# Kernel optimization log

Hardware: AMD Instinct MI355X
Metric: run time of the kernel (lower is better)

Reference implementation:

```python
import jax, jax.numpy as jnp
import numpy as np

N = 10000
E = 320000
F_IN = 512
NHID = 32
LATENT = 16


def setup_inputs() -> dict:
    key = jax.random.key(0)
    k1, k2, k3, k4, k5 = jax.random.split(key, 5)
    x = jax.random.normal(k1, (N, F_IN), dtype=jnp.float32)
    W1 = jax.random.normal(k2, (F_IN, NHID), dtype=jnp.float32) * (1.0 / np.sqrt(F_IN))
    W2 = jax.random.normal(k3, (NHID, LATENT), dtype=jnp.float32) * (1.0 / np.sqrt(NHID))
    edge_index = jax.random.randint(k4, (2, E), 0, N, dtype=jnp.int32)
    edge_weight = jax.random.uniform(k5, (E,), dtype=jnp.float32)
    return {"x": x, "W1": W1, "W2": W2, "edge_index": edge_index,
            "edge_weight": edge_weight}


def _spmm(edge_index, edge_weight, h):
    # out[dst] += w * h[src]  (sparse normalized-adjacency matmul)
    src, dst = edge_index[0], edge_index[1]
    msgs = edge_weight[:, None] * h[src]          # [E, D] gather + scale
    return jax.ops.segment_sum(msgs, dst, num_segments=N)  # [N, D]


def reference(x, W1, W2, edge_index, edge_weight):
    # GCNConv layer 1: adj @ (x @ W1)
    h = _spmm(edge_index, edge_weight, x @ W1)    # [N, NHID]
    # GCNConv layer 2: adj @ (h @ W2)
    z = _spmm(edge_index, edge_weight, h @ W2)    # [N, LATENT]
    # Inner-product decoder: sigmoid(z @ z^T)
    adj_recon = jax.nn.sigmoid(z @ z.T)           # [N, N]
    return adj_recon, z
```

## Files before the change

### kernel.cpp

```cpp
#include <hip/hip_runtime.h>
#include <cstdint>
#include <cstddef>

#define N_NODES 10000
#define F_IN    512
#define NHID    32
#define LATENT  16

__global__ __launch_bounds__(256) void gemm1_kernel(const float* __restrict__ x,
                                                    const float* __restrict__ W1,
                                                    float* __restrict__ h0) {
    __shared__ float xs[8][F_IN];
    const int row0 = blockIdx.x * 8;
    for (int t = threadIdx.x; t < 8 * F_IN; t += 256) {
        const int r = t >> 9;
        const int c = t & (F_IN - 1);
        if (row0 + r < N_NODES)
            xs[r][c] = x[(size_t)(row0 + r) * F_IN + c];
    }
    __syncthreads();

    const int col = threadIdx.x & 31;
    const int r   = threadIdx.x >> 5;
    if (row0 + r < N_NODES) {
        float acc = 0.f;
#pragma unroll 8
        for (int k = 0; k < F_IN; ++k) {
            acc += xs[r][k] * W1[k * NHID + col];
        }
        h0[(size_t)(row0 + r) * NHID + col] = acc;
    }
}

template <int D>
__global__ __launch_bounds__(256) void spmm_kernel(const int* __restrict__ src,
                                                   const int* __restrict__ dst,
                                                   const float* __restrict__ w,
                                                   const float* __restrict__ hin,
                                                   float* __restrict__ hout,
                                                   int E) {
    const int idx = blockIdx.x * 256 + threadIdx.x;
    const int e = idx / D;
    const int d = idx & (D - 1);
    if (e < E) {
        const int s = src[e];
        const int t = dst[e];
        const float val = w[e] * hin[(size_t)s * D + d];
        atomicAdd(&hout[(size_t)t * D + d], val);
    }
}

__global__ __launch_bounds__(256) void gemm2_kernel(const float* __restrict__ h,
                                                    const float* __restrict__ W2,
                                                    float* __restrict__ z0) {
    __shared__ float w2s[NHID * LATENT];
    for (int t = threadIdx.x; t < NHID * LATENT; t += 256) w2s[t] = W2[t];
    __syncthreads();

    const int idx = blockIdx.x * 256 + threadIdx.x;
    if (idx < N_NODES * LATENT) {
        const int row = idx >> 4;
        const int col = idx & (LATENT - 1);
        const float* __restrict__ hr = h + (size_t)row * NHID;
        float acc = 0.f;
#pragma unroll
        for (int k = 0; k < NHID; ++k) acc += hr[k] * w2s[k * LATENT + col];
        z0[idx] = acc;
    }
}

#define TI 32

__device__ __forceinline__ float sigmoid_fast(float x) {
    return __builtin_amdgcn_rcpf(1.0f + __expf(-x));
}

__global__ __launch_bounds__(256) void decoder_kernel(const float* __restrict__ z,
                                                      float* __restrict__ out) {
    const int j  = blockIdx.x * 256 + threadIdx.x;
    const int i0 = blockIdx.y * TI;

    float4 zj0, zj1, zj2, zj3;
    if (j < N_NODES) {
        const float4* __restrict__ zp = (const float4*)(z + (size_t)j * LATENT);
        zj0 = zp[0]; zj1 = zp[1]; zj2 = zp[2]; zj3 = zp[3];
    } else {
        zj0 = zj1 = zj2 = zj3 = make_float4(0.f, 0.f, 0.f, 0.f);
    }

    const int imax = min(TI, N_NODES - i0);
    if (imax == TI) {
#pragma unroll 4
        for (int ii = 0; ii < TI; ++ii) {
            const float4* __restrict__ zi = (const float4*)(z + (size_t)(i0 + ii) * LATENT);
            const float4 a0 = zi[0], a1 = zi[1], a2 = zi[2], a3 = zi[3];
            float acc = a0.x * zj0.x + a0.y * zj0.y + a0.z * zj0.z + a0.w * zj0.w
                      + a1.x * zj1.x + a1.y * zj1.y + a1.z * zj1.z + a1.w * zj1.w
                      + a2.x * zj2.x + a2.y * zj2.y + a2.z * zj2.z + a2.w * zj2.w
                      + a3.x * zj3.x + a3.y * zj3.y + a3.z * zj3.z + a3.w * zj3.w;
            if (j < N_NODES) {
                __builtin_nontemporal_store(sigmoid_fast(acc),
                                            &out[(size_t)(i0 + ii) * N_NODES + j]);
            }
        }
    } else {
        for (int ii = 0; ii < imax; ++ii) {
            const float4* __restrict__ zi = (const float4*)(z + (size_t)(i0 + ii) * LATENT);
            const float4 a0 = zi[0], a1 = zi[1], a2 = zi[2], a3 = zi[3];
            float acc = a0.x * zj0.x + a0.y * zj0.y + a0.z * zj0.z + a0.w * zj0.w
                      + a1.x * zj1.x + a1.y * zj1.y + a1.z * zj1.z + a1.w * zj1.w
                      + a2.x * zj2.x + a2.y * zj2.y + a2.z * zj2.z + a2.w * zj2.w
                      + a3.x * zj3.x + a3.y * zj3.y + a3.z * zj3.z + a3.w * zj3.w;
            if (j < N_NODES) {
                __builtin_nontemporal_store(sigmoid_fast(acc),
                                            &out[(size_t)(i0 + ii) * N_NODES + j]);
            }
        }
    }
}

extern "C" void kernel_launch(void* const* d_in, const int* in_sizes, int n_in,
                              void* d_out, int out_size, void* d_ws, size_t ws_size,
                              hipStream_t stream) {
    const float* x  = (const float*)d_in[0];
    const float* W1 = (const float*)d_in[1];
    const float* W2 = (const float*)d_in[2];
    const int*   ei = (const int*)d_in[3];
    const float* ew = (const float*)d_in[4];
    const int E = in_sizes[3] / 2;
    const int* src = ei;
    const int* dst = ei + E;

    float* out = (float*)d_out;
    float* z   = out + (size_t)N_NODES * N_NODES;

    float* h0 = out;
    float* h  = h0 + N_NODES * NHID;
    float* z0 = h  + N_NODES * NHID;

    hipMemsetAsync(h, 0, (size_t)N_NODES * NHID * sizeof(float), stream);
    hipMemsetAsync(z, 0, (size_t)N_NODES * LATENT * sizeof(float), stream);

    gemm1_kernel<<<(N_NODES + 7) / 8, 256, 0, stream>>>(x, W1, h0);
    spmm_kernel<NHID><<<(E * NHID + 255) / 256, 256, 0, stream>>>(src, dst, ew, h0, h, E);

    gemm2_kernel<<<(N_NODES * LATENT + 255) / 256, 256, 0, stream>>>(h, W2, z0);
    spmm_kernel<LATENT><<<(E * LATENT + 255) / 256, 256, 0, stream>>>(src, dst, ew, z0, z, E);

    dim3 dgrid((N_NODES + 255) / 256, (N_NODES + TI - 1) / TI);
    decoder_kernel<<<dgrid, 256, 0, stream>>>(z, out);
}
```

Before: 507.9 us.

## Fold memsets into gemm1, vectorize decoder stores to four columns per thread

Removes the two hipMemsetAsync calls and zeroes the spmm accumulators inside gemm1, using one thread per element across the 1250 blocks. gemm1 now reads x from shared memory as float4 and keeps four independent accumulators. The decoder computes four output columns per thread and writes them with one 128-bit nontemporal store per row, which cuts per-thread z_i loads and store instructions for the dominant 400MB output write. Bounds checks are dropped because N is divisible by 8 and by 4.

```diff
diff --git a/kernel.cpp b/kernel.cpp
--- a/kernel.cpp
+++ b/kernel.cpp
@@ -7,29 +7,38 @@
 #define NHID    32
 #define LATENT  16
 
+typedef float v4f __attribute__((ext_vector_type(4)));
+
 __global__ __launch_bounds__(256) void gemm1_kernel(const float* __restrict__ x,
                                                     const float* __restrict__ W1,
-                                                    float* __restrict__ h0) {
+                                                    float* __restrict__ h0,
+                                                    float* __restrict__ h,
+                                                    float* __restrict__ z) {
+    const int gid = blockIdx.x * 256 + threadIdx.x;
+    h[gid] = 0.f;
+    if (gid < N_NODES * LATENT) z[gid] = 0.f;
+
     __shared__ float xs[8][F_IN];
     const int row0 = blockIdx.x * 8;
     for (int t = threadIdx.x; t < 8 * F_IN; t += 256) {
         const int r = t >> 9;
         const int c = t & (F_IN - 1);
-        if (row0 + r < N_NODES)
-            xs[r][c] = x[(size_t)(row0 + r) * F_IN + c];
+        xs[r][c] = x[(size_t)(row0 + r) * F_IN + c];
     }
     __syncthreads();
 
     const int col = threadIdx.x & 31;
     const int r   = threadIdx.x >> 5;
-    if (row0 + r < N_NODES) {
-        float acc = 0.f;
-#pragma unroll 8
-        for (int k = 0; k < F_IN; ++k) {
-            acc += xs[r][k] * W1[k * NHID + col];
-        }
-        h0[(size_t)(row0 + r) * NHID + col] = acc;
+    float a0 = 0.f, a1 = 0.f, a2 = 0.f, a3 = 0.f;
+#pragma unroll 4
+    for (int k = 0; k < F_IN; k += 4) {
+        const float4 xv = *(const float4*)&xs[r][k];
+        a0 += xv.x * W1[(k + 0) * NHID + col];
+        a1 += xv.y * W1[(k + 1) * NHID + col];
+        a2 += xv.z * W1[(k + 2) * NHID + col];
+        a3 += xv.w * W1[(k + 3) * NHID + col];
     }
+    h0[(size_t)(row0 + r) * NHID + col] = (a0 + a1) + (a2 + a3);
 }
 
 template <int D>
@@ -77,45 +86,53 @@
 
 __global__ __launch_bounds__(256) void decoder_kernel(const float* __restrict__ z,
                                                       float* __restrict__ out) {
-    const int j  = blockIdx.x * 256 + threadIdx.x;
+    const int j0 = (blockIdx.x * 256 + threadIdx.x) << 2;
     const int i0 = blockIdx.y * TI;
+    if (j0 >= N_NODES) return;
 
-    float4 zj0, zj1, zj2, zj3;
-    if (j < N_NODES) {
-        const float4* __restrict__ zp = (const float4*)(z + (size_t)j * LATENT);
-        zj0 = zp[0]; zj1 = zp[1]; zj2 = zp[2]; zj3 = zp[3];
-    } else {
-        zj0 = zj1 = zj2 = zj3 = make_float4(0.f, 0.f, 0.f, 0.f);
+    float4 zj0[4], zj1[4], zj2[4], zj3[4];
+    {
+        const float4* zp0 = (const float4*)(z + (size_t)(j0 + 0) * LATENT);
+        const float4* zp1 = (const float4*)(z + (size_t)(j0 + 1) * LATENT);
+        const float4* zp2 = (const float4*)(z + (size_t)(j0 + 2) * LATENT);
+        const float4* zp3 = (const float4*)(z + (size_t)(j0 + 3) * LATENT);
+#pragma unroll
+        for (int p = 0; p < 4; ++p) {
+            zj0[p] = zp0[p]; zj1[p] = zp1[p]; zj2[p] = zp2[p]; zj3[p] = zp3[p];
+        }
     }
 
     const int imax = min(TI, N_NODES - i0);
-    if (imax == TI) {
-#pragma unroll 4
-        for (int ii = 0; ii < TI; ++ii) {
-            const float4* __restrict__ zi = (const float4*)(z + (size_t)(i0 + ii) * LATENT);
-            const float4 a0 = zi[0], a1 = zi[1], a2 = zi[2], a3 = zi[3];
-            float acc = a0.x * zj0.x + a0.y * zj0.y + a0.z * zj0.z + a0.w * zj0.w
-                      + a1.x * zj1.x + a1.y * zj1.y + a1.z * zj1.z + a1.w * zj1.w
-                      + a2.x * zj2.x + a2.y * zj2.y + a2.z * zj2.z + a2.w * zj2.w
-                      + a3.x * zj3.x + a3.y * zj3.y + a3.z * zj3.z + a3.w * zj3.w;
-            if (j < N_NODES) {
-                __builtin_nontemporal_store(sigmoid_fast(acc),
-                                            &out[(size_t)(i0 + ii) * N_NODES + j]);
-            }
-        }
-    } else {
-        for (int ii = 0; ii < imax; ++ii) {
-            const float4* __restrict__ zi = (const float4*)(z + (size_t)(i0 + ii) * LATENT);
-            const float4 a0 = zi[0], a1 = zi[1], a2 = zi[2], a3 = zi[3];
-            float acc = a0.x * zj0.x + a0.y * zj0.y + a0.z * zj0.z + a0.w * zj0.w
-                      + a1.x * zj1.x + a1.y * zj1.y + a1.z * zj1.z + a1.w * zj1.w
-                      + a2.x * zj2.x + a2.y * zj2.y + a2.z * zj2.z + a2.w * zj2.w
-                      + a3.x * zj3.x + a3.y * zj3.y + a3.z * zj3.z + a3.w * zj3.w;
-            if (j < N_NODES) {
-                __builtin_nontemporal_store(sigmoid_fast(acc),
-                                            &out[(size_t)(i0 + ii) * N_NODES + j]);
-            }
-        }
+#pragma unroll 2
+    for (int ii = 0; ii < imax; ++ii) {
+        const float4* __restrict__ zi = (const float4*)(z + (size_t)(i0 + ii) * LATENT);
+        const float4 a0 = zi[0], a1 = zi[1], a2 = zi[2], a3 = zi[3];
+
+        v4f r;
+        r.x = a0.x*zj0[0].x + a0.y*zj0[0].y + a0.z*zj0[0].z + a0.w*zj0[0].w
+            + a1.x*zj0[1].x + a1.y*zj0[1].y + a1.z*zj0[1].z + a1.w*zj0[1].w
+            + a2.x*zj0[2].x + a2.y*zj0[2].y + a2.z*zj0[2].z + a2.w*zj0[2].w
+            + a3.x*zj0[3].x + a3.y*zj0[3].y + a3.z*zj0[3].z + a3.w*zj0[3].w;
+        r.y = a0.x*zj1[0].x + a0.y*zj1[0].y + a0.z*zj1[0].z + a0.w*zj1[0].w
+            + a1.x*zj1[1].x + a1.y*zj1[1].y + a1.z*zj1[1].z + a1.w*zj1[1].w
+            + a2.x*zj1[2].x + a2.y*zj1[2].y + a2.z*zj1[2].z + a2.w*zj1[2].w
+            + a3.x*zj1[3].x + a3.y*zj1[3].y + a3.z*zj1[3].z + a3.w*zj1[3].w;
+        r.z = a0.x*zj2[0].x + a0.y*zj2[0].y + a0.z*zj2[0].z + a0.w*zj2[0].w
+            + a1.x*zj2[1].x + a1.y*zj2[1].y + a1.z*zj2[1].z + a1.w*zj2[1].w
+            + a2.x*zj2[2].x + a2.y*zj2[2].y + a2.z*zj2[2].z + a2.w*zj2[2].w
+            + a3.x*zj2[3].x + a3.y*zj2[3].y + a3.z*zj2[3].z + a3.w*zj2[3].w;
+        r.w = a0.x*zj3[0].x + a0.y*zj3[0].y + a0.z*zj3[0].z + a0.w*zj3[0].w
+            + a1.x*zj3[1].x + a1.y*zj3[1].y + a1.z*zj3[1].z + a1.w*zj3[1].w
+            + a2.x*zj3[2].x + a2.y*zj3[2].y + a2.z*zj3[2].z + a2.w*zj3[2].w
+            + a3.x*zj3[3].x + a3.y*zj3[3].y + a3.z*zj3[3].z + a3.w*zj3[3].w;
+
+        r.x = sigmoid_fast(r.x);
+        r.y = sigmoid_fast(r.y);
+        r.z = sigmoid_fast(r.z);
+        r.w = sigmoid_fast(r.w);
+
+        __builtin_nontemporal_store(
+            r, (v4f*)(out + (size_t)(i0 + ii) * N_NODES + j0));
     }
 }
 
@@ -138,15 +155,12 @@
     float* h  = h0 + N_NODES * NHID;
     float* z0 = h  + N_NODES * NHID;
 
-    hipMemsetAsync(h, 0, (size_t)N_NODES * NHID * sizeof(float), stream);
-    hipMemsetAsync(z, 0, (size_t)N_NODES * LATENT * sizeof(float), stream);
-
-    gemm1_kernel<<<(N_NODES + 7) / 8, 256, 0, stream>>>(x, W1, h0);
+    gemm1_kernel<<<N_NODES / 8, 256, 0, stream>>>(x, W1, h0, h, z);
     spmm_kernel<NHID><<<(E * NHID + 255) / 256, 256, 0, stream>>>(src, dst, ew, h0, h, E);
 
     gemm2_kernel<<<(N_NODES * LATENT + 255) / 256, 256, 0, stream>>>(h, W2, z0);
     spmm_kernel<LATENT><<<(E * LATENT + 255) / 256, 256, 0, stream>>>(src, dst, ew, z0, z, E);
 
-    dim3 dgrid((N_NODES + 255) / 256, (N_NODES + TI - 1) / TI);
+    dim3 dgrid((N_NODES / 4 + 255) / 256, (N_NODES + TI - 1) / TI);
     decoder_kernel<<<dgrid, 256, 0, stream>>>(z, out);
 }
```

After: 502.7 us. Within noise of the previous version (-1.0%).
